# Kernel tuning notes

Measured on AMD Instinct MI355X. Metric: run time of the kernel, lower is better.

Reference implementation:

```python
import jax, jax.numpy as jnp
import numpy as np

H = 16
D_MODEL = 1024
DK = D_MODEL // H

def setup_inputs() -> dict:
    key = jax.random.key(0)
    ks = jax.random.split(key, 9)
    B, S = 4, 2048
    s = 1.0 / np.sqrt(D_MODEL)
    inp = {
        'X': jax.random.normal(ks[0], (B, S, D_MODEL), dtype=jnp.float32),
        'Wq': jax.random.uniform(ks[1], (D_MODEL, D_MODEL), jnp.float32, -s, s),
        'bq': jax.random.uniform(ks[2], (D_MODEL,), jnp.float32, -s, s),
        'Wk': jax.random.uniform(ks[3], (D_MODEL, D_MODEL), jnp.float32, -s, s),
        'bk': jax.random.uniform(ks[4], (D_MODEL,), jnp.float32, -s, s),
        'Wv': jax.random.uniform(ks[5], (D_MODEL, D_MODEL), jnp.float32, -s, s),
        'bv': jax.random.uniform(ks[6], (D_MODEL,), jnp.float32, -s, s),
        'Wo': jax.random.uniform(ks[7], (D_MODEL, D_MODEL), jnp.float32, -s, s),
        'bo': jax.random.uniform(ks[8], (D_MODEL,), jnp.float32, -s, s),
    }
    return inp

def reference(X, Wq, bq, Wk, bk, Wv, bv, Wo, bo):
    B, S, _ = X.shape
    # projections (torch Linear: x @ W.T + b)
    def proj(W, b):
        y = X @ W.T + b                      # [B,S,D]
        return y.reshape(B, S, H, DK).transpose(0, 2, 1, 3)  # [B,H,S,DK]
    q = proj(Wq, bq)
    k = proj(Wk, bk)
    v = proj(Wv, bv)
    scores = jnp.einsum('bhsd,bhtd->bhst', q, k) / jnp.sqrt(jnp.float32(DK))
    attn = jax.nn.softmax(scores, axis=-1)
    out = jnp.einsum('bhst,bhtd->bhsd', attn, v)  # [B,H,S,DK]
    out = out.transpose(0, 2, 1, 3).reshape(B, S, D_MODEL)
    return out @ Wo.T + bo
```

## Files before the change

### kernel.cpp

```cpp
#include <hip/hip_runtime.h>
#include <hip/hip_bf16.h>

#define DEVI __device__ __forceinline__

typedef __bf16 bf16x8_t __attribute__((ext_vector_type(8)));
typedef float f32x4_t __attribute__((ext_vector_type(4)));
typedef unsigned int u32;
typedef unsigned short u16;

DEVI u16 f2bf(float f) {
  u32 u = __builtin_bit_cast(u32, f);
  u = (u + 0x7fffu + ((u >> 16) & 1u)) >> 16;
  return (u16)u;
}

DEVI void gload_lds16(const void* g, void* l) {
  __builtin_amdgcn_global_load_lds((const __attribute__((address_space(1))) u32*)g,
                                   (__attribute__((address_space(3))) u32*)l, 16, 0, 0);
}

__global__ void cvt_kernel(const float* __restrict__ src, u16* __restrict__ dst, int n4) {
  int i = blockIdx.x * blockDim.x + threadIdx.x;
  int stride = gridDim.x * blockDim.x;
  for (; i < n4; i += stride) {
    float4 f = reinterpret_cast<const float4*>(src)[i];
    ushort4 o;
    o.x = f2bf(f.x); o.y = f2bf(f.y); o.z = f2bf(f.z); o.w = f2bf(f.w);
    reinterpret_cast<ushort4*>(dst)[i] = o;
  }
}

__global__ void cvt4_kernel(const float* __restrict__ s0, const float* __restrict__ s1,
                            const float* __restrict__ s2, const float* __restrict__ s3,
                            u16* __restrict__ w0, u16* __restrict__ w1,
                            u16* __restrict__ w2, u16* __restrict__ w3, int n4) {
  const float* src = (blockIdx.y == 0) ? s0 : (blockIdx.y == 1) ? s1 : (blockIdx.y == 2) ? s2 : s3;
  u16* dst = (blockIdx.y == 0) ? w0 : (blockIdx.y == 1) ? w1 : (blockIdx.y == 2) ? w2 : w3;
  int i = blockIdx.x * blockDim.x + threadIdx.x;
  int stride = gridDim.x * blockDim.x;
  for (; i < n4; i += stride) {
    float4 f = reinterpret_cast<const float4*>(src)[i];
    ushort4 o;
    o.x = f2bf(f.x); o.y = f2bf(f.y); o.z = f2bf(f.z); o.w = f2bf(f.w);
    reinterpret_cast<ushort4*>(dst)[i] = o;
  }
}

DEVI void stage_tile32(const u16* __restrict__ g, int ldg, u16* lds, int wid, int lane) {
#pragma unroll
  for (int i = 0; i < 2; ++i) {
    int idx = wid * 128 + i * 64 + lane;
    int row = idx >> 2, seg = idx & 3;
    gload_lds16(g + row * ldg + seg * 8, lds + (wid * 128 + i * 64) * 8);
  }
}

DEVI void gemm_mainloop(const u16* __restrict__ A, const u16* __restrict__ W, int Kdim,
                        int m0, int n0, int wid, int lane,
                        u16 (*As)[128 * 32], u16 (*Bs)[128 * 32], f32x4_t acc[4][4]) {
#pragma unroll
  for (int m = 0; m < 4; ++m)
#pragma unroll
    for (int n = 0; n < 4; ++n)
#pragma unroll
      for (int r = 0; r < 4; ++r) acc[m][n][r] = 0.f;

  const int NK = Kdim >> 5;
  stage_tile32(A + m0 * Kdim, Kdim, As[0], wid, lane);
  stage_tile32(W + n0 * Kdim, Kdim, Bs[0], wid, lane);
  __syncthreads();

  const int wr = wid >> 1, wc = wid & 1;
  const int r16 = lane & 15, koff = (lane >> 4) * 8;
  for (int kt = 0; kt < NK; ++kt) {
    int cur = kt & 1;
    if (kt + 1 < NK) {
      stage_tile32(A + m0 * Kdim + (kt + 1) * 32, Kdim, As[cur ^ 1], wid, lane);
      stage_tile32(W + n0 * Kdim + (kt + 1) * 32, Kdim, Bs[cur ^ 1], wid, lane);
    }
    bf16x8_t af[4], bf[4];
#pragma unroll
    for (int m = 0; m < 4; ++m)
      af[m] = *reinterpret_cast<const bf16x8_t*>(&As[cur][(wr * 64 + m * 16 + r16) * 32 + koff]);
#pragma unroll
    for (int n = 0; n < 4; ++n)
      bf[n] = *reinterpret_cast<const bf16x8_t*>(&Bs[cur][(wc * 64 + n * 16 + r16) * 32 + koff]);
#pragma unroll
    for (int m = 0; m < 4; ++m)
#pragma unroll
      for (int n = 0; n < 4; ++n)
        acc[m][n] = __builtin_amdgcn_mfma_f32_16x16x32_bf16(af[m], bf[n], acc[m][n], 0, 0, 0);
    __syncthreads();
  }
}

__global__ __launch_bounds__(256) void qkv_gemm(
    const u16* __restrict__ Xb,
    const u16* __restrict__ Wqb, const u16* __restrict__ Wkb, const u16* __restrict__ Wvb,
    const float* __restrict__ bq, const float* __restrict__ bk, const float* __restrict__ bv,
    u16* __restrict__ Qo, u16* __restrict__ Ko, u16* __restrict__ Vto) {
  __shared__ u16 As[2][128 * 32];
  __shared__ u16 Bs[2][128 * 32];
  const int tid = threadIdx.x, lane = tid & 63, wid = tid >> 6;
  const int z = blockIdx.z;
  const u16* W = (z == 0) ? Wqb : (z == 1) ? Wkb : Wvb;
  const float* bias = (z == 0) ? bq : (z == 1) ? bk : bv;
  const int m0 = blockIdx.y * 128, n0 = blockIdx.x * 128;

  f32x4_t acc[4][4];
  gemm_mainloop(Xb, W, 1024, m0, n0, wid, lane, As, Bs, acc);

  const int wr = wid >> 1, wc = wid & 1;
  const int rbase = m0 + wr * 64 + ((lane >> 4) << 2);
#pragma unroll
  for (int n = 0; n < 4; ++n) {
    int col = n0 + wc * 64 + n * 16 + (lane & 15);
    float bia = bias[col];
    int h = col >> 6, d = col & 63;
#pragma unroll
    for (int m = 0; m < 4; ++m) {
      int row0 = rbase + m * 16;
      int b = row0 >> 11, s0 = row0 & 2047;
      int bh = b * 16 + h;
      if (z == 2) {
        ushort4 pk;
        pk.x = f2bf(acc[m][n][0] + bia);
        pk.y = f2bf(acc[m][n][1] + bia);
        pk.z = f2bf(acc[m][n][2] + bia);
        pk.w = f2bf(acc[m][n][3] + bia);
        *reinterpret_cast<ushort4*>(&Vto[bh * 131072 + d * 2048 + s0]) = pk;
      } else {
        u16* P = (z == 0) ? Qo : Ko;
        float sc = (z == 0) ? 0.125f : 1.0f;
#pragma unroll
        for (int r = 0; r < 4; ++r)
          P[bh * 131072 + (s0 + r) * 64 + d] = f2bf((acc[m][n][r] + bia) * sc);
      }
    }
  }
}

__global__ __launch_bounds__(256) void attn_kernel(const u16* __restrict__ Qb,
                                                   const u16* __restrict__ Kb,
                                                   const u16* __restrict__ Vtb,
                                                   u16* __restrict__ Ob) {
  __shared__ u16 Ks[64 * 64];
  __shared__ u16 Vs[64 * 64];
  __shared__ u16 Ps[4][32 * 64];
  const int tid = threadIdx.x, lane = tid & 63, wid = tid >> 6;
  const int bh = blockIdx.y;
  const int b = bh >> 4, h = bh & 15;
  const u16* Qh = Qb + bh * 131072;
  const u16* Kh = Kb + bh * 131072;
  const u16* Vh = Vtb + bh * 131072;
  const int q0 = blockIdx.x * 128 + wid * 32;
  const int r16 = lane & 15, g4 = lane >> 4;

  bf16x8_t qf[2][2];
#pragma unroll
  for (int mt = 0; mt < 2; ++mt)
#pragma unroll
    for (int kk = 0; kk < 2; ++kk)
      qf[mt][kk] = *reinterpret_cast<const bf16x8_t*>(
          &Qh[(q0 + mt * 16 + r16) * 64 + kk * 32 + g4 * 8]);

  f32x4_t oacc[2][4];
  float rl[2][4];
#pragma unroll
  for (int mt = 0; mt < 2; ++mt) {
#pragma unroll
    for (int dt = 0; dt < 4; ++dt)
#pragma unroll
      for (int r = 0; r < 4; ++r) oacc[mt][dt][r] = 0.f;
#pragma unroll
    for (int r = 0; r < 4; ++r) rl[mt][r] = 0.f;
  }

  char* KsB = (char*)Ks;
  char* VsB = (char*)Vs;
  char* PsB = (char*)&Ps[wid][0];

  for (int t0 = 0; t0 < 2048; t0 += 64) {
#pragma unroll
    for (int i = 0; i < 2; ++i) {
      int idx = wid * 128 + i * 64 + lane;
      int row = idx >> 3, seg = idx & 7;
      int sseg = seg ^ (row & 7);
      gload_lds16(Kh + (t0 + row) * 64 + sseg * 8, Ks + (wid * 128 + i * 64) * 8);
      gload_lds16(Vh + row * 2048 + t0 + sseg * 8, Vs + (wid * 128 + i * 64) * 8);
    }
    __syncthreads();

    f32x4_t sacc[2][4];
#pragma unroll
    for (int mt = 0; mt < 2; ++mt)
#pragma unroll
      for (int nt = 0; nt < 4; ++nt)
#pragma unroll
        for (int r = 0; r < 4; ++r) sacc[mt][nt][r] = 0.f;
#pragma unroll
    for (int nt = 0; nt < 4; ++nt) {
      int row = nt * 16 + r16;
#pragma unroll
      for (int kk = 0; kk < 2; ++kk) {
        int bo_ = (row * 128 + kk * 64 + g4 * 16) ^ ((row & 7) << 4);
        bf16x8_t kf = *reinterpret_cast<const bf16x8_t*>(KsB + bo_);
#pragma unroll
        for (int mt = 0; mt < 2; ++mt)
          sacc[mt][nt] = __builtin_amdgcn_mfma_f32_16x16x32_bf16(qf[mt][kk], kf, sacc[mt][nt], 0, 0, 0);
      }
    }

#pragma unroll
    for (int mt = 0; mt < 2; ++mt)
#pragma unroll
      for (int nt = 0; nt < 4; ++nt)
#pragma unroll
        for (int r = 0; r < 4; ++r) {
          float p = __builtin_amdgcn_exp2f(sacc[mt][nt][r] * 1.44269504f);
          rl[mt][r] += p;
          int prow = mt * 16 + g4 * 4 + r;
          int bo_ = (prow * 128 + (nt * 16 + r16) * 2) ^ ((prow & 7) << 4);
          *(u16*)(PsB + bo_) = f2bf(p);
        }

    bf16x8_t pf[2][2];
#pragma unroll
    for (int mt = 0; mt < 2; ++mt)
#pragma unroll
      for (int kk = 0; kk < 2; ++kk) {
        int prow = mt * 16 + r16;
        int bo_ = (prow * 128 + kk * 64 + g4 * 16) ^ ((prow & 7) << 4);
        pf[mt][kk] = *reinterpret_cast<const bf16x8_t*>(PsB + bo_);
      }
#pragma unroll
    for (int dt = 0; dt < 4; ++dt) {
      int drow = dt * 16 + r16;
#pragma unroll
      for (int kk = 0; kk < 2; ++kk) {
        int bo_ = (drow * 128 + kk * 64 + g4 * 16) ^ ((drow & 7) << 4);
        bf16x8_t vf = *reinterpret_cast<const bf16x8_t*>(VsB + bo_);
#pragma unroll
        for (int mt = 0; mt < 2; ++mt)
          oacc[mt][dt] = __builtin_amdgcn_mfma_f32_16x16x32_bf16(pf[mt][kk], vf, oacc[mt][dt], 0, 0, 0);
      }
    }
    __syncthreads();
  }

#pragma unroll
  for (int mt = 0; mt < 2; ++mt) {
    float rinv[4];
#pragma unroll
    for (int r = 0; r < 4; ++r) {
      float s = rl[mt][r];
      s += __shfl_xor(s, 1, 16);
      s += __shfl_xor(s, 2, 16);
      s += __shfl_xor(s, 4, 16);
      s += __shfl_xor(s, 8, 16);
      rinv[r] = 1.0f / s;
    }
#pragma unroll
    for (int dt = 0; dt < 4; ++dt) {
      int d = dt * 16 + r16;
#pragma unroll
      for (int r = 0; r < 4; ++r) {
        int srow = q0 + mt * 16 + g4 * 4 + r;
        Ob[(b * 2048 + srow) * 1024 + h * 64 + d] = f2bf(oacc[mt][dt][r] * rinv[r]);
      }
    }
  }
}

__global__ __launch_bounds__(256) void out_gemm(const u16* __restrict__ Ob,
                                                const u16* __restrict__ Wob,
                                                const float* __restrict__ bo,
                                                float* __restrict__ out) {
  __shared__ u16 As[2][128 * 32];
  __shared__ u16 Bs[2][128 * 32];
  const int tid = threadIdx.x, lane = tid & 63, wid = tid >> 6;
  const int m0 = blockIdx.y * 128, n0 = blockIdx.x * 128;
  f32x4_t acc[4][4];
  gemm_mainloop(Ob, Wob, 1024, m0, n0, wid, lane, As, Bs, acc);
  const int wr = wid >> 1, wc = wid & 1;
#pragma unroll
  for (int n = 0; n < 4; ++n) {
    int col = n0 + wc * 64 + n * 16 + (lane & 15);
    float bia = bo[col];
#pragma unroll
    for (int m = 0; m < 4; ++m) {
      int row0 = m0 + wr * 64 + m * 16 + ((lane >> 4) << 2);
#pragma unroll
      for (int r = 0; r < 4; ++r) out[(row0 + r) * 1024 + col] = acc[m][n][r] + bia;
    }
  }
}

extern "C" void kernel_launch(void* const* d_in, const int* in_sizes, int n_in,
                              void* d_out, int out_size, void* d_ws, size_t ws_size,
                              hipStream_t stream) {
  const float* X  = (const float*)d_in[0];
  const float* Wq = (const float*)d_in[1];
  const float* bq = (const float*)d_in[2];
  const float* Wk = (const float*)d_in[3];
  const float* bk = (const float*)d_in[4];
  const float* Wv = (const float*)d_in[5];
  const float* bv = (const float*)d_in[6];
  const float* Wo = (const float*)d_in[7];
  const float* bo = (const float*)d_in[8];
  float* out = (float*)d_out;

  char* ws = (char*)d_ws;
  u16* Xb  = (u16*)(ws + 0);
  u16* Ob  = (u16*)(ws + 0);
  u16* Wqb = (u16*)(ws + 16777216);
  u16* Wkb = (u16*)(ws + 18874368);
  u16* Wvb = (u16*)(ws + 20971520);
  u16* Wob = (u16*)(ws + 23068672);
  u16* Qb  = (u16*)(ws + 25165824);
  u16* Kb  = (u16*)(ws + 41943040);
  u16* Vtb = (u16*)(ws + 58720256);

  hipLaunchKernelGGL(cvt_kernel, dim3(2048), dim3(256), 0, stream, X, Xb, 2097152);
  hipLaunchKernelGGL(cvt4_kernel, dim3(256, 4), dim3(256), 0, stream,
                     Wq, Wk, Wv, Wo, Wqb, Wkb, Wvb, Wob, 262144);

  hipLaunchKernelGGL(qkv_gemm, dim3(8, 64, 3), dim3(256), 0, stream,
                     Xb, Wqb, Wkb, Wvb, bq, bk, bv, Qb, Kb, Vtb);
  hipLaunchKernelGGL(attn_kernel, dim3(16, 64), dim3(256), 0, stream, Qb, Kb, Vtb, Ob);
  hipLaunchKernelGGL(out_gemm, dim3(8, 64), dim3(256), 0, stream, Ob, Wob, bo, out);
}
```

Measured before the change: 347.0 us.

## Keep softmax probabilities in registers, double-buffer K/V tiles, remap attention grid

The QK^T MFMA now swaps its operand order so the score fragment layout matches the PV A-operand. That lets the exponentiated probabilities be packed straight into bf16 registers instead of round-tripping through LDS. V^T columns are permuted in the QKV epilogue to match that packing, and log2(e) is folded into the Q scale. K/V tiles are double-buffered so the next load overlaps compute, and a 1D grid remaps blocks across heads for better L2/XCD locality. The trade-offs are packing correctness risk from the column permutation and a cruder round-to-nearest bf16 conversion.

```diff
diff --git a/kernel.cpp b/kernel.cpp
--- a/kernel.cpp
+++ b/kernel.cpp
@@ -6,6 +6,7 @@
 typedef __bf16 bf16x8_t __attribute__((ext_vector_type(8)));
 typedef float f32x4_t __attribute__((ext_vector_type(4)));
 typedef unsigned int u32;
+typedef u32 u32x4_t __attribute__((ext_vector_type(4)));
 typedef unsigned short u16;
 
 DEVI u16 f2bf(float f) {
@@ -128,10 +129,13 @@
         pk.y = f2bf(acc[m][n][1] + bia);
         pk.z = f2bf(acc[m][n][2] + bia);
         pk.w = f2bf(acc[m][n][3] + bia);
-        *reinterpret_cast<ushort4*>(&Vto[bh * 131072 + d * 2048 + s0]) = pk;
+        int cv = (s0 >> 2) & 15;
+        int cs = ((cv >> 3) << 3) | ((cv & 3) << 1) | ((cv >> 2) & 1);
+        int s0p = (s0 & ~63) | (cs << 2);
+        *reinterpret_cast<ushort4*>(&Vto[bh * 131072 + d * 2048 + s0p]) = pk;
       } else {
         u16* P = (z == 0) ? Qo : Ko;
-        float sc = (z == 0) ? 0.125f : 1.0f;
+        float sc = (z == 0) ? 0.18033688f : 1.0f;
 #pragma unroll
         for (int r = 0; r < 4; ++r)
           P[bh * 131072 + (s0 + r) * 64 + d] = f2bf((acc[m][n][r] + bia) * sc);
@@ -144,16 +148,17 @@
                                                    const u16* __restrict__ Kb,
                                                    const u16* __restrict__ Vtb,
                                                    u16* __restrict__ Ob) {
-  __shared__ u16 Ks[64 * 64];
-  __shared__ u16 Vs[64 * 64];
-  __shared__ u16 Ps[4][32 * 64];
+  __shared__ u16 Ks[2][64 * 64];
+  __shared__ u16 Vs[2][64 * 64];
   const int tid = threadIdx.x, lane = tid & 63, wid = tid >> 6;
-  const int bh = blockIdx.y;
+  const int bid = blockIdx.x;
+  const int bh = (bid & 7) * 8 + (bid >> 7);
+  const int qt = (bid >> 3) & 15;
   const int b = bh >> 4, h = bh & 15;
   const u16* Qh = Qb + bh * 131072;
   const u16* Kh = Kb + bh * 131072;
   const u16* Vh = Vtb + bh * 131072;
-  const int q0 = blockIdx.x * 128 + wid * 32;
+  const int q0 = qt * 128 + wid * 32;
   const int r16 = lane & 15, g4 = lane >> 4;
 
   bf16x8_t qf[2][2];
@@ -165,31 +170,36 @@
           &Qh[(q0 + mt * 16 + r16) * 64 + kk * 32 + g4 * 8]);
 
   f32x4_t oacc[2][4];
-  float rl[2][4];
-#pragma unroll
-  for (int mt = 0; mt < 2; ++mt) {
+  float rl[2] = {0.f, 0.f};
+#pragma unroll
+  for (int mt = 0; mt < 2; ++mt)
 #pragma unroll
     for (int dt = 0; dt < 4; ++dt)
 #pragma unroll
       for (int r = 0; r < 4; ++r) oacc[mt][dt][r] = 0.f;
-#pragma unroll
-    for (int r = 0; r < 4; ++r) rl[mt][r] = 0.f;
-  }
-
-  char* KsB = (char*)Ks;
-  char* VsB = (char*)Vs;
-  char* PsB = (char*)&Ps[wid][0];
-
-  for (int t0 = 0; t0 < 2048; t0 += 64) {
-#pragma unroll
-    for (int i = 0; i < 2; ++i) {
-      int idx = wid * 128 + i * 64 + lane;
-      int row = idx >> 3, seg = idx & 7;
-      int sseg = seg ^ (row & 7);
-      gload_lds16(Kh + (t0 + row) * 64 + sseg * 8, Ks + (wid * 128 + i * 64) * 8);
-      gload_lds16(Vh + row * 2048 + t0 + sseg * 8, Vs + (wid * 128 + i * 64) * 8);
-    }
-    __syncthreads();
+
+#define ATTN_STAGE(buf, t_)                                                     \
+  {                                                                             \
+    _Pragma("unroll") for (int i = 0; i < 2; ++i) {                             \
+      int idx = wid * 128 + i * 64 + lane;                                      \
+      int row = idx >> 3, seg = idx & 7;                                        \
+      int sseg = seg ^ (row & 7);                                               \
+      gload_lds16(Kh + ((t_) * 64 + row) * 64 + sseg * 8,                       \
+                  (u16*)Ks[buf] + (wid * 128 + i * 64) * 8);                    \
+      gload_lds16(Vh + row * 2048 + (t_) * 64 + sseg * 8,                       \
+                  (u16*)Vs[buf] + (wid * 128 + i * 64) * 8);                    \
+    }                                                                           \
+  }
+
+  ATTN_STAGE(0, 0)
+  __syncthreads();
+
+  for (int t = 0; t < 32; ++t) {
+    int cur = t & 1;
+    if (t + 1 < 32) ATTN_STAGE(cur ^ 1, t + 1)
+
+    const char* KsB = (const char*)Ks[cur];
+    const char* VsB = (const char*)Vs[cur];
 
     f32x4_t sacc[2][4];
 #pragma unroll
@@ -207,32 +217,34 @@
         bf16x8_t kf = *reinterpret_cast<const bf16x8_t*>(KsB + bo_);
 #pragma unroll
         for (int mt = 0; mt < 2; ++mt)
-          sacc[mt][nt] = __builtin_amdgcn_mfma_f32_16x16x32_bf16(qf[mt][kk], kf, sacc[mt][nt], 0, 0, 0);
-      }
-    }
-
-#pragma unroll
-    for (int mt = 0; mt < 2; ++mt)
-#pragma unroll
-      for (int nt = 0; nt < 4; ++nt)
-#pragma unroll
-        for (int r = 0; r < 4; ++r) {
-          float p = __builtin_amdgcn_exp2f(sacc[mt][nt][r] * 1.44269504f);
-          rl[mt][r] += p;
-          int prow = mt * 16 + g4 * 4 + r;
-          int bo_ = (prow * 128 + (nt * 16 + r16) * 2) ^ ((prow & 7) << 4);
-          *(u16*)(PsB + bo_) = f2bf(p);
-        }
-
-    bf16x8_t pf[2][2];
-#pragma unroll
-    for (int mt = 0; mt < 2; ++mt)
-#pragma unroll
-      for (int kk = 0; kk < 2; ++kk) {
-        int prow = mt * 16 + r16;
-        int bo_ = (prow * 128 + kk * 64 + g4 * 16) ^ ((prow & 7) << 4);
-        pf[mt][kk] = *reinterpret_cast<const bf16x8_t*>(PsB + bo_);
-      }
+          sacc[mt][nt] = __builtin_amdgcn_mfma_f32_16x16x32_bf16(kf, qf[mt][kk], sacc[mt][nt], 0, 0, 0);
+      }
+    }
+
+    bf16x8_t pfr[2][2];
+#pragma unroll
+    for (int mt = 0; mt < 2; ++mt) {
+      u32 dw[8];
+#pragma unroll
+      for (int nt = 0; nt < 4; ++nt) {
+        float e0 = __builtin_amdgcn_exp2f(sacc[mt][nt][0]);
+        float e1 = __builtin_amdgcn_exp2f(sacc[mt][nt][1]);
+        float e2 = __builtin_amdgcn_exp2f(sacc[mt][nt][2]);
+        float e3 = __builtin_amdgcn_exp2f(sacc[mt][nt][3]);
+        rl[mt] += (e0 + e1) + (e2 + e3);
+        u32 u0 = __builtin_bit_cast(u32, e0) + 0x8000u;
+        u32 u1 = __builtin_bit_cast(u32, e1) + 0x8000u;
+        u32 u2 = __builtin_bit_cast(u32, e2) + 0x8000u;
+        u32 u3 = __builtin_bit_cast(u32, e3) + 0x8000u;
+        dw[nt * 2]     = (u0 >> 16) | (u1 & 0xffff0000u);
+        dw[nt * 2 + 1] = (u2 >> 16) | (u3 & 0xffff0000u);
+      }
+      u32x4_t lo = {dw[0], dw[1], dw[2], dw[3]};
+      u32x4_t hi = {dw[4], dw[5], dw[6], dw[7]};
+      pfr[mt][0] = __builtin_bit_cast(bf16x8_t, lo);
+      pfr[mt][1] = __builtin_bit_cast(bf16x8_t, hi);
+    }
+
 #pragma unroll
     for (int dt = 0; dt < 4; ++dt) {
       int drow = dt * 16 + r16;
@@ -242,7 +254,7 @@
         bf16x8_t vf = *reinterpret_cast<const bf16x8_t*>(VsB + bo_);
 #pragma unroll
         for (int mt = 0; mt < 2; ++mt)
-          oacc[mt][dt] = __builtin_amdgcn_mfma_f32_16x16x32_bf16(pf[mt][kk], vf, oacc[mt][dt], 0, 0, 0);
+          oacc[mt][dt] = __builtin_amdgcn_mfma_f32_16x16x32_bf16(pfr[mt][kk], vf, oacc[mt][dt], 0, 0, 0);
       }
     }
     __syncthreads();
@@ -250,16 +262,12 @@
 
 #pragma unroll
   for (int mt = 0; mt < 2; ++mt) {
+    float s = rl[mt];
+    s += __shfl_xor(s, 16);
+    s += __shfl_xor(s, 32);
     float rinv[4];
 #pragma unroll
-    for (int r = 0; r < 4; ++r) {
-      float s = rl[mt][r];
-      s += __shfl_xor(s, 1, 16);
-      s += __shfl_xor(s, 2, 16);
-      s += __shfl_xor(s, 4, 16);
-      s += __shfl_xor(s, 8, 16);
-      rinv[r] = 1.0f / s;
-    }
+    for (int r = 0; r < 4; ++r) rinv[r] = 1.0f / __shfl(s, g4 * 4 + r, 16);
 #pragma unroll
     for (int dt = 0; dt < 4; ++dt) {
       int d = dt * 16 + r16;
@@ -327,6 +335,6 @@
 
   hipLaunchKernelGGL(qkv_gemm, dim3(8, 64, 3), dim3(256), 0, stream,
                      Xb, Wqb, Wkb, Wvb, bq, bk, bv, Qb, Kb, Vtb);
-  hipLaunchKernelGGL(attn_kernel, dim3(16, 64), dim3(256), 0, stream, Qb, Kb, Vtb, Ob);
+  hipLaunchKernelGGL(attn_kernel, dim3(1024), dim3(256), 0, stream, Qb, Kb, Vtb, Ob);
   hipLaunchKernelGGL(out_gemm, dim3(8, 64), dim3(256), 0, stream, Ob, Wob, bo, out);
 }
```

New measurement: 317.8 us. 1.09x faster.
